# Kernel tuning notes

Measured on AMD Instinct MI355X. Metric: run time of the kernel, lower is better.

## Reference

```python
import jax, jax.numpy as jnp
import numpy as np

N = 100000
E = 1600000
IN_C = 128
HID_C = 128
OUT_C = 128


def sage_conv(x, edge_index, W_l, b_l, W_r):
    # PyG SAGEConv (mean aggr): out = mean_{j in N(i)} x_j @ W_l^T + b_l + x_i @ W_r^T
    src, dst = edge_index[0], edge_index[1]
    n = x.shape[0]
    msgs = x[src]                                            # [E, d] gather
    summed = jax.ops.segment_sum(msgs, dst, num_segments=n)  # [N, d]
    deg = jax.ops.segment_sum(jnp.ones((src.shape[0],), x.dtype), dst, num_segments=n)
    mean = summed / jnp.maximum(deg, 1.0)[:, None]
    return mean @ W_l.T + b_l + x @ W_r.T


def setup_inputs() -> dict:
    key = jax.random.key(0)
    ks = jax.random.split(key, 8)
    x = jax.random.normal(ks[0], (N, IN_C), dtype=jnp.float32)
    edge_index = jax.random.randint(ks[1], (2, E), 0, N, dtype=jnp.int64)
    s1 = 1.0 / np.sqrt(IN_C)
    s2 = 1.0 / np.sqrt(HID_C)
    W1_l = jax.random.uniform(ks[2], (HID_C, IN_C), jnp.float32, -s1, s1)
    b1 = jax.random.uniform(ks[3], (HID_C,), jnp.float32, -s1, s1)
    W1_r = jax.random.uniform(ks[4], (HID_C, IN_C), jnp.float32, -s1, s1)
    W2_l = jax.random.uniform(ks[5], (OUT_C, HID_C), jnp.float32, -s2, s2)
    b2 = jax.random.uniform(ks[6], (OUT_C,), jnp.float32, -s2, s2)
    W2_r = jax.random.uniform(ks[7], (OUT_C, HID_C), jnp.float32, -s2, s2)
    return {"x": x, "edge_index": edge_index, "W1_l": W1_l, "b1": b1, "W1_r": W1_r,
            "W2_l": W2_l, "b2": b2, "W2_r": W2_r}


def reference(x, edge_index, W1_l, b1, W1_r, W2_l, b2, W2_r):
    h = sage_conv(x, edge_index, W1_l, b1, W1_r)
    h = jax.nn.relu(h)
    # F.dropout(p=0.4, training=self.training): identity in eval mode
    out = sage_conv(h, edge_index, W2_l, b2, W2_r)
    return out
```

## Files before the change

kernel.cpp:

```cpp
#include <hip/hip_runtime.h>

#define N_NODES 100000
#define N_EDGES 1600000
#define C 128
#define SCAN_B 1024
#define LDW 264

#define BSH 7
#define NBUCK 782
#define BCAP 2560
#define TILE1 8192
#define NBLK1 196

typedef __attribute__((ext_vector_type(8))) short bfrag;
typedef __attribute__((ext_vector_type(4))) float f32x4;

__device__ __forceinline__ ushort f2b(float x) {
    uint u = __builtin_bit_cast(uint, x);
    u += 0x7fffu + ((u >> 16) & 1u);
    return (ushort)(u >> 16);
}
__device__ __forceinline__ float b2f(ushort b) {
    uint u = ((uint)b) << 16;
    return __builtin_bit_cast(float, u);
}


__global__ __launch_bounds__(256) void bucket_scatter2_k(
        const int* __restrict__ ei, uint* __restrict__ buck, int* __restrict__ bcur) {
    __shared__ int hist[NBUCK];
    __shared__ int base_l[NBUCK];
    int t = threadIdx.x;
    int tile0 = blockIdx.x * TILE1;

    for (int i = t; i < NBUCK; i += 256) hist[i] = 0;
    __syncthreads();
    #pragma unroll 4
    for (int j = 0; j < TILE1 / 256; ++j) {
        int e = tile0 + j * 256 + t;
        if (e < N_EDGES) atomicAdd(&hist[ei[N_EDGES + e] >> BSH], 1);
    }
    __syncthreads();
    for (int i = t; i < NBUCK; i += 256) {
        int h = hist[i];
        base_l[i] = h ? atomicAdd(&bcur[i], h) : 0;
    }
    __syncthreads();
    for (int i = t; i < NBUCK; i += 256) hist[i] = 0;
    __syncthreads();
    #pragma unroll 4
    for (int j = 0; j < TILE1 / 256; ++j) {
        int e = tile0 + j * 256 + t;
        if (e < N_EDGES) {
            int src = ei[e];
            int dst = ei[N_EDGES + e];
            int b = dst >> BSH;
            int r = base_l[b] + atomicAdd(&hist[b], 1);
            if (r < BCAP) buck[(uint)b * BCAP + r] = (uint)src | ((uint)(dst & 127) << 17);
        }
    }
}

__global__ __launch_bounds__(256) void bucket_hist2_k(
        const uint* __restrict__ buck, const int* __restrict__ bcur, int* __restrict__ deg) {
    __shared__ int cnt_l[128];
    int b = blockIdx.x, t = threadIdx.x;
    if (t < 128) cnt_l[t] = 0;
    __syncthreads();
    int cnt = min(bcur[b], BCAP);
    const uint* bp = buck + (uint)b * BCAP;
    for (int i = t; i < cnt; i += 256) atomicAdd(&cnt_l[bp[i] >> 17], 1);
    __syncthreads();
    int node = (b << BSH) + t;
    if (t < 128 && node < N_NODES) deg[node] = cnt_l[t];
}

__global__ void scan1_k(const int* __restrict__ deg, int* __restrict__ rowptr,
                        int* __restrict__ bsums) {
    __shared__ int s[256];
    int b = blockIdx.x, t = threadIdx.x;
    int base = b * SCAN_B + t * 4;
    int v[4];
    int sum = 0;
    #pragma unroll
    for (int j = 0; j < 4; ++j) {
        int idx = base + j;
        v[j] = (idx < N_NODES) ? deg[idx] : 0;
        sum += v[j];
    }
    s[t] = sum;
    __syncthreads();
    for (int off = 1; off < 256; off <<= 1) {
        int x = (t >= off) ? s[t - off] : 0;
        __syncthreads();
        s[t] += x;
        __syncthreads();
    }
    int run = (t > 0) ? s[t - 1] : 0;
    #pragma unroll
    for (int j = 0; j < 4; ++j) {
        run += v[j];
        int idx = base + j;
        if (idx < N_NODES) rowptr[idx + 1] = run;
    }
    if (t == 255) bsums[b] = s[255];
}

__global__ void scan2_k(int* __restrict__ bsums, int nb) {
    __shared__ int s[128];
    int t = threadIdx.x;
    s[t] = (t < nb) ? bsums[t] : 0;
    __syncthreads();
    for (int off = 1; off < 128; off <<= 1) {
        int x = (t >= off) ? s[t - off] : 0;
        __syncthreads();
        s[t] += x;
        __syncthreads();
    }
    if (t < nb) bsums[t] = (t > 0) ? s[t - 1] : 0;
}

__global__ void scan3_k(int* __restrict__ rowptr, const int* __restrict__ bsums) {
    int i = blockIdx.x * blockDim.x + threadIdx.x;
    if (i < N_NODES) rowptr[i + 1] += bsums[i / SCAN_B];
    if (i == 0) rowptr[0] = 0;
}

__global__ __launch_bounds__(256) void bucket_place2_k(
        const uint* __restrict__ buck, const int* __restrict__ bcur,
        const int* __restrict__ rowptr, int* __restrict__ col) {
    __shared__ int base_n[129];
    __shared__ int fill_l[128];
    __shared__ int col_l[BCAP];
    int b = blockIdx.x, t = threadIdx.x;
    int node0 = b << BSH;
    if (t <= 128) base_n[t] = rowptr[min(node0 + t, N_NODES)];
    if (t < 128) fill_l[t] = 0;
    __syncthreads();
    int pbase = base_n[0];
    int cnt = min(bcur[b], BCAP);
    const uint* bp = buck + (uint)b * BCAP;
    for (int i = t; i < cnt; i += 256) {
        uint p = bp[i];
        int rel = p >> 17;
        int pos = base_n[rel] + atomicAdd(&fill_l[rel], 1) - pbase;
        if (pos < BCAP) col_l[pos] = (int)(p & 0x1FFFFu);
    }
    __syncthreads();
    int total = min(base_n[128] - pbase, BCAP);
    for (int i = t; i < total; i += 256) col[pbase + i] = col_l[i];
}


__global__ void cast_x_k(const float4* __restrict__ in, ushort4* __restrict__ out) {
    int i = blockIdx.x * blockDim.x + threadIdx.x;
    if (i < N_NODES * C / 4) {
        float4 v = in[i];
        ushort4 o = { f2b(v.x), f2b(v.y), f2b(v.z), f2b(v.w) };
        out[i] = o;
    }
}

__global__ void wprep_k(const float* __restrict__ Wl, const float* __restrict__ Wr,
                        ushort* __restrict__ wcat) {
    int i = blockIdx.x * blockDim.x + threadIdx.x;
    int o = i >> 8, k = i & 255;
    float v = (k < 128) ? Wl[o * 128 + k] : Wr[o * 128 + (k - 128)];
    wcat[i] = f2b(v);
}

__global__ __launch_bounds__(256) void agg_bf16_k(
        const uint* __restrict__ feat,
        uint* __restrict__ outb,
        const int* __restrict__ rowptr, const int* __restrict__ col) {
    int wave = threadIdx.x >> 6, lane = threadIdx.x & 63;
    int node = blockIdx.x * 4 + wave;
    int beg = rowptr[node], end = rowptr[node + 1];
    float a0 = 0.f, a1 = 0.f;
    for (int e0 = beg; e0 < end; e0 += 64) {
        int cnt = min(64, end - e0);
        int cv = col[min(e0 + lane, end - 1)];
        int j = 0;
        for (; j + 8 <= cnt; j += 8) {
            uint v0 = feat[((uint)__shfl(cv, j + 0) << 6) + lane];
            uint v1 = feat[((uint)__shfl(cv, j + 1) << 6) + lane];
            uint v2 = feat[((uint)__shfl(cv, j + 2) << 6) + lane];
            uint v3 = feat[((uint)__shfl(cv, j + 3) << 6) + lane];
            uint v4 = feat[((uint)__shfl(cv, j + 4) << 6) + lane];
            uint v5 = feat[((uint)__shfl(cv, j + 5) << 6) + lane];
            uint v6 = feat[((uint)__shfl(cv, j + 6) << 6) + lane];
            uint v7 = feat[((uint)__shfl(cv, j + 7) << 6) + lane];
            a0 += b2f((ushort)v0) + b2f((ushort)v1) + b2f((ushort)v2) + b2f((ushort)v3)
                + b2f((ushort)v4) + b2f((ushort)v5) + b2f((ushort)v6) + b2f((ushort)v7);
            a1 += b2f((ushort)(v0 >> 16)) + b2f((ushort)(v1 >> 16))
                + b2f((ushort)(v2 >> 16)) + b2f((ushort)(v3 >> 16))
                + b2f((ushort)(v4 >> 16)) + b2f((ushort)(v5 >> 16))
                + b2f((ushort)(v6 >> 16)) + b2f((ushort)(v7 >> 16));
        }
        for (; j < cnt; ++j) {
            uint v = feat[((uint)__shfl(cv, j) << 6) + lane];
            a0 += b2f((ushort)v);
            a1 += b2f((ushort)(v >> 16));
        }
    }
    float inv = 1.f / (float)max(end - beg, 1);
    uint o = (uint)f2b(a0 * inv) | ((uint)f2b(a1 * inv) << 16);
    outb[((uint)node << 6) + lane] = o;
}

template <bool RELU, bool OUT_BF16>
__global__ __launch_bounds__(256) void mfma_lin_k(
        const ushort* __restrict__ A0,
        const ushort* __restrict__ A1,
        const ushort* __restrict__ W,
        const float* __restrict__ bias,
        void* __restrict__ outp) {
    __shared__ ushort wl[128 * LDW];
    int t = threadIdx.x;

    const bfrag* wg = (const bfrag*)W;
    #pragma unroll
    for (int j = 0; j < 16; ++j) {
        int p = t + j * 256;
        int o = p >> 5, kb = p & 31;
        *(bfrag*)&wl[o * LDW + kb * 8] = wg[p];
    }
    __syncthreads();

    int wave = t >> 6, lane = t & 63;
    int g = lane >> 4, r16 = lane & 15;
    long base = (long)blockIdx.x * 128 + wave * 32;

    const ushort* a0p[2];
    const ushort* a1p[2];
    #pragma unroll
    for (int mt = 0; mt < 2; ++mt) {
        long mrow = base + mt * 16 + r16;
        if (mrow >= N_NODES) mrow = N_NODES - 1;
        a0p[mt] = A0 + mrow * C + g * 8;
        a1p[mt] = A1 + mrow * C + g * 8;
    }

    f32x4 acc[2][8];
    #pragma unroll
    for (int mt = 0; mt < 2; ++mt)
        #pragma unroll
        for (int nt = 0; nt < 8; ++nt) acc[mt][nt] = (f32x4){0.f, 0.f, 0.f, 0.f};

    #pragma unroll
    for (int c = 0; c < 8; ++c) {
        bfrag a[2];
        #pragma unroll
        for (int mt = 0; mt < 2; ++mt)
            a[mt] = (c < 4) ? *(const bfrag*)(a0p[mt] + c * 32)
                            : *(const bfrag*)(a1p[mt] + (c - 4) * 32);
        #pragma unroll
        for (int nt = 0; nt < 8; ++nt) {
            bfrag b = *(const bfrag*)&wl[(nt * 16 + r16) * LDW + g * 8 + c * 32];
            acc[0][nt] = __builtin_amdgcn_mfma_f32_16x16x32_bf16(a[0], b, acc[0][nt], 0, 0, 0);
            acc[1][nt] = __builtin_amdgcn_mfma_f32_16x16x32_bf16(a[1], b, acc[1][nt], 0, 0, 0);
        }
    }

    #pragma unroll
    for (int nt = 0; nt < 8; ++nt) {
        int o = nt * 16 + r16;
        float bv = bias[o];
        #pragma unroll
        for (int mt = 0; mt < 2; ++mt) {
            #pragma unroll
            for (int i = 0; i < 4; ++i) {
                long orow = base + mt * 16 + g * 4 + i;
                if (orow < N_NODES) {
                    float v = acc[mt][nt][i] + bv;
                    if (RELU) v = fmaxf(v, 0.f);
                    if (OUT_BF16)
                        ((ushort*)outp)[orow * C + o] = f2b(v);
                    else
                        ((float*)outp)[orow * C + o] = v;
                }
            }
        }
    }
}

extern "C" void kernel_launch(void* const* d_in, const int* in_sizes, int n_in,
                              void* d_out, int out_size, void* d_ws, size_t ws_size,
                              hipStream_t stream) {
    const float* x   = (const float*)d_in[0];
    const int* ei    = (const int*)d_in[1];
    const float* W1l = (const float*)d_in[2];
    const float* b1  = (const float*)d_in[3];
    const float* W1r = (const float*)d_in[4];
    const float* W2l = (const float*)d_in[5];
    const float* b2  = (const float*)d_in[6];
    const float* W2r = (const float*)d_in[7];
    float* out       = (float*)d_out;

    char* ws = (char*)d_ws;
    size_t off = 0;
    ushort* xb    = (ushort*)(ws + off); off += (size_t)N_NODES * C * 2;
    ushort* aggb  = (ushort*)(ws + off); off += (size_t)N_NODES * C * 2;
    ushort* hb    = (ushort*)(ws + off); off += (size_t)N_NODES * C * 2;
    uint* buck    = (uint*)hb;
    ushort* wcat1 = (ushort*)(ws + off); off += (size_t)C * 256 * 2;
    ushort* wcat2 = (ushort*)(ws + off); off += (size_t)C * 256 * 2;
    int* col      = (int*)(ws + off);    off += (size_t)N_EDGES * 4;
    int* rowptr   = (int*)(ws + off);    off += (size_t)(N_NODES + 1) * 4;
    int* deg      = (int*)(ws + off);    off += (size_t)NBUCK * 128 * 4;
    int* bcur     = (int*)(ws + off);    off += 1024 * 4;
    int* bsums    = (int*)(ws + off);    off += 1024 * 4;

    int nb = (N_NODES + SCAN_B - 1) / SCAN_B;

    hipMemsetAsync(bcur, 0, 1024 * 4, stream);
    bucket_scatter2_k<<<NBLK1, 256, 0, stream>>>(ei, buck, bcur);
    bucket_hist2_k<<<NBUCK, 256, 0, stream>>>(buck, bcur, deg);
    scan1_k<<<nb, 256, 0, stream>>>(deg, rowptr, bsums);
    scan2_k<<<1, 128, 0, stream>>>(bsums, nb);
    scan3_k<<<(N_NODES + 255) / 256, 256, 0, stream>>>(rowptr, bsums);
    bucket_place2_k<<<NBUCK, 256, 0, stream>>>(buck, bcur, rowptr, col);

    cast_x_k<<<(N_NODES * C / 4 + 255) / 256, 256, 0, stream>>>((const float4*)x, (ushort4*)xb);
    wprep_k<<<128, 256, 0, stream>>>(W1l, W1r, wcat1);
    wprep_k<<<128, 256, 0, stream>>>(W2l, W2r, wcat2);

    int lin_blocks = (N_NODES + 127) / 128;

    agg_bf16_k<<<N_NODES / 4, 256, 0, stream>>>((const uint*)xb, (uint*)aggb, rowptr, col);
    mfma_lin_k<true, true><<<lin_blocks, 256, 0, stream>>>(aggb, xb, wcat1, b1, hb);

    agg_bf16_k<<<N_NODES / 4, 256, 0, stream>>>((const uint*)hb, (uint*)aggb, rowptr, col);
    mfma_lin_k<false, false><<<lin_blocks, 256, 0, stream>>>(aggb, hb, wcat2, b2, out);
}
```

Before: 260.3 us.

## Split bf16 features into 8 column slabs so gathers stay cache-resident

Stores node features in a slab-major layout of eight 16-column slices, each 32 bytes per node, and runs aggregation once per slab. Each wave now gathers 8 neighbors at a time with 8 lanes per row, then reduces with cross-lane shuffles. The intent is for each slab's working set (about 3.2 MB) to fit in L2, so random neighbor gathers hit cache instead of HBM. In exchange there are 8x more blocks, col and rowptr are re-read once per slab, each gather is a short 32-byte segment, and the MFMA linear kernel has to read and write the new layout.

```diff
diff --git a/kernel.cpp b/kernel.cpp
--- a/kernel.cpp
+++ b/kernel.cpp
@@ -24,6 +24,7 @@
     uint u = ((uint)b) << 16;
     return __builtin_bit_cast(float, u);
 }
+
 
 
 __global__ __launch_bounds__(256) void bucket_scatter2_k(
@@ -152,12 +153,14 @@
 }
 
 
-__global__ void cast_x_k(const float4* __restrict__ in, ushort4* __restrict__ out) {
+__global__ void cast_x_sm_k(const float* __restrict__ in, uint* __restrict__ out) {
     int i = blockIdx.x * blockDim.x + threadIdx.x;
-    if (i < N_NODES * C / 4) {
-        float4 v = in[i];
-        ushort4 o = { f2b(v.x), f2b(v.y), f2b(v.z), f2b(v.w) };
-        out[i] = o;
+    if (i < N_NODES * 64) {
+        int s = i / (N_NODES * 8);
+        int rem = i - s * (N_NODES * 8);
+        int n = rem >> 3, u = rem & 7;
+        const float* p = in + n * C + s * 16 + u * 2;
+        out[i] = (uint)f2b(p[0]) | ((uint)f2b(p[1]) << 16);
     }
 }
 
@@ -169,49 +172,44 @@
     wcat[i] = f2b(v);
 }
 
-__global__ __launch_bounds__(256) void agg_bf16_k(
+__global__ __launch_bounds__(256) void agg_sm_k(
         const uint* __restrict__ feat,
         uint* __restrict__ outb,
         const int* __restrict__ rowptr, const int* __restrict__ col) {
     int wave = threadIdx.x >> 6, lane = threadIdx.x & 63;
-    int node = blockIdx.x * 4 + wave;
+    int s = blockIdx.x & 7;
+    int node = (blockIdx.x >> 3) * 4 + wave;
+    const uint* fs = feat + ((uint)s * N_NODES << 3);
     int beg = rowptr[node], end = rowptr[node + 1];
+    int grp = lane >> 3, u = lane & 7;
     float a0 = 0.f, a1 = 0.f;
     for (int e0 = beg; e0 < end; e0 += 64) {
-        int cnt = min(64, end - e0);
-        int cv = col[min(e0 + lane, end - 1)];
-        int j = 0;
-        for (; j + 8 <= cnt; j += 8) {
-            uint v0 = feat[((uint)__shfl(cv, j + 0) << 6) + lane];
-            uint v1 = feat[((uint)__shfl(cv, j + 1) << 6) + lane];
-            uint v2 = feat[((uint)__shfl(cv, j + 2) << 6) + lane];
-            uint v3 = feat[((uint)__shfl(cv, j + 3) << 6) + lane];
-            uint v4 = feat[((uint)__shfl(cv, j + 4) << 6) + lane];
-            uint v5 = feat[((uint)__shfl(cv, j + 5) << 6) + lane];
-            uint v6 = feat[((uint)__shfl(cv, j + 6) << 6) + lane];
-            uint v7 = feat[((uint)__shfl(cv, j + 7) << 6) + lane];
-            a0 += b2f((ushort)v0) + b2f((ushort)v1) + b2f((ushort)v2) + b2f((ushort)v3)
-                + b2f((ushort)v4) + b2f((ushort)v5) + b2f((ushort)v6) + b2f((ushort)v7);
-            a1 += b2f((ushort)(v0 >> 16)) + b2f((ushort)(v1 >> 16))
-                + b2f((ushort)(v2 >> 16)) + b2f((ushort)(v3 >> 16))
-                + b2f((ushort)(v4 >> 16)) + b2f((ushort)(v5 >> 16))
-                + b2f((ushort)(v6 >> 16)) + b2f((ushort)(v7 >> 16));
+        int cv = __builtin_nontemporal_load(&col[min(e0 + lane, end - 1)]);
+        int nit = min(64, end - e0);
+        for (int it = 0; it < nit; it += 16) {
+            int i0 = it + grp, i1 = it + 8 + grp;
+            int s0 = __shfl(cv, i0);
+            int s1 = __shfl(cv, i1);
+            uint f0 = fs[((uint)s0 << 3) + u];
+            uint f1 = fs[((uint)s1 << 3) + u];
+            if (i0 < nit) { a0 += b2f((ushort)f0); a1 += b2f((ushort)(f0 >> 16)); }
+            if (i1 < nit) { a0 += b2f((ushort)f1); a1 += b2f((ushort)(f1 >> 16)); }
         }
-        for (; j < cnt; ++j) {
-            uint v = feat[((uint)__shfl(cv, j) << 6) + lane];
-            a0 += b2f((ushort)v);
-            a1 += b2f((ushort)(v >> 16));
-        }
-    }
-    float inv = 1.f / (float)max(end - beg, 1);
-    uint o = (uint)f2b(a0 * inv) | ((uint)f2b(a1 * inv) << 16);
-    outb[((uint)node << 6) + lane] = o;
+    }
+    a0 += __shfl_xor(a0, 8);  a1 += __shfl_xor(a1, 8);
+    a0 += __shfl_xor(a0, 16); a1 += __shfl_xor(a1, 16);
+    a0 += __shfl_xor(a0, 32); a1 += __shfl_xor(a1, 32);
+    if (lane < 8) {
+        float inv = 1.f / (float)max(end - beg, 1);
+        uint o = (uint)f2b(a0 * inv) | ((uint)f2b(a1 * inv) << 16);
+        __builtin_nontemporal_store(o, &outb[(((uint)s * N_NODES + (uint)node) << 3) + u]);
+    }
 }
 
 template <bool RELU, bool OUT_BF16>
 __global__ __launch_bounds__(256) void mfma_lin_k(
-        const ushort* __restrict__ A0,
-        const ushort* __restrict__ A1,
+        const uint* __restrict__ A0,
+        const uint* __restrict__ A1,
         const ushort* __restrict__ W,
         const float* __restrict__ bias,
         void* __restrict__ outp) {
@@ -231,15 +229,15 @@
     int g = lane >> 4, r16 = lane & 15;
     long base = (long)blockIdx.x * 128 + wave * 32;
 
-    const ushort* a0p[2];
-    const ushort* a1p[2];
+    uint mr[2];
     #pragma unroll
     for (int mt = 0; mt < 2; ++mt) {
         long mrow = base + mt * 16 + r16;
         if (mrow >= N_NODES) mrow = N_NODES - 1;
-        a0p[mt] = A0 + mrow * C + g * 8;
-        a1p[mt] = A1 + mrow * C + g * 8;
-    }
+        mr[mt] = (uint)mrow;
+    }
+    uint su = (uint)(g >> 1);
+    uint u0 = (uint)(g & 1) * 4;
 
     f32x4 acc[2][8];
     #pragma unroll
@@ -249,11 +247,12 @@
 
     #pragma unroll
     for (int c = 0; c < 8; ++c) {
+        const uint* bp = (c < 4) ? A0 : A1;
+        uint sidx = (uint)(c < 4 ? 2 * c : 2 * (c - 4)) + su;
         bfrag a[2];
         #pragma unroll
         for (int mt = 0; mt < 2; ++mt)
-            a[mt] = (c < 4) ? *(const bfrag*)(a0p[mt] + c * 32)
-                            : *(const bfrag*)(a1p[mt] + (c - 4) * 32);
+            a[mt] = *(const bfrag*)(bp + (((sidx * N_NODES + mr[mt]) << 3) + u0));
         #pragma unroll
         for (int nt = 0; nt < 8; ++nt) {
             bfrag b = *(const bfrag*)&wl[(nt * 16 + r16) * LDW + g * 8 + c * 32];
@@ -275,7 +274,7 @@
                     float v = acc[mt][nt][i] + bv;
                     if (RELU) v = fmaxf(v, 0.f);
                     if (OUT_BF16)
-                        ((ushort*)outp)[orow * C + o] = f2b(v);
+                        ((ushort*)outp)[(((uint)nt * N_NODES + (uint)orow) << 4) + r16] = f2b(v);
                     else
                         ((float*)outp)[orow * C + o] = v;
                 }
@@ -299,10 +298,10 @@
 
     char* ws = (char*)d_ws;
     size_t off = 0;
-    ushort* xb    = (ushort*)(ws + off); off += (size_t)N_NODES * C * 2;
-    ushort* aggb  = (ushort*)(ws + off); off += (size_t)N_NODES * C * 2;
-    ushort* hb    = (ushort*)(ws + off); off += (size_t)N_NODES * C * 2;
-    uint* buck    = (uint*)hb;
+    uint* xb      = (uint*)(ws + off);   off += (size_t)N_NODES * C * 2;
+    uint* aggb    = (uint*)(ws + off);   off += (size_t)N_NODES * C * 2;
+    uint* hb      = (uint*)(ws + off);   off += (size_t)N_NODES * C * 2;
+    uint* buck    = hb;
     ushort* wcat1 = (ushort*)(ws + off); off += (size_t)C * 256 * 2;
     ushort* wcat2 = (ushort*)(ws + off); off += (size_t)C * 256 * 2;
     int* col      = (int*)(ws + off);    off += (size_t)N_EDGES * 4;
@@ -321,15 +320,16 @@
     scan3_k<<<(N_NODES + 255) / 256, 256, 0, stream>>>(rowptr, bsums);
     bucket_place2_k<<<NBUCK, 256, 0, stream>>>(buck, bcur, rowptr, col);
 
-    cast_x_k<<<(N_NODES * C / 4 + 255) / 256, 256, 0, stream>>>((const float4*)x, (ushort4*)xb);
+    cast_x_sm_k<<<(N_NODES * 64 + 255) / 256, 256, 0, stream>>>(x, xb);
     wprep_k<<<128, 256, 0, stream>>>(W1l, W1r, wcat1);
     wprep_k<<<128, 256, 0, stream>>>(W2l, W2r, wcat2);
 
     int lin_blocks = (N_NODES + 127) / 128;
-
-    agg_bf16_k<<<N_NODES / 4, 256, 0, stream>>>((const uint*)xb, (uint*)aggb, rowptr, col);
+    int agg_blocks = (N_NODES / 4) * 8;
+
+    agg_sm_k<<<agg_blocks, 256, 0, stream>>>(xb, aggb, rowptr, col);
     mfma_lin_k<true, true><<<lin_blocks, 256, 0, stream>>>(aggb, xb, wcat1, b1, hb);
 
-    agg_bf16_k<<<N_NODES / 4, 256, 0, stream>>>((const uint*)hb, (uint*)aggb, rowptr, col);
+    agg_sm_k<<<agg_blocks, 256, 0, stream>>>(hb, aggb, rowptr, col);
     mfma_lin_k<false, false><<<lin_blocks, 256, 0, stream>>>(aggb, hb, wcat2, b2, out);
 }
```

Result: slower. 587.0 us (+125.5%).

## Aggregate neighbor features via MFMA with one-hot selection matrices over 16-node groups

Applied to the files above, without the earlier changes.

Each wave now handles 16 consecutive destination nodes. It gathers their combined edge list in chunks of 32, stages the neighbor rows transposed in LDS, and sums them with bf16 MFMA against a one-hot matrix that marks each edge's destination row. The local destination index is packed into the upper bits of col during CSR placement so the wave can build that matrix. The aim is to replace per-lane scalar bf16 unpack-and-add work with matrix instructions and to use wider gathers. The cost is more LDS traffic and transposes, and wasted MFMA work on the zero entries of the one-hot matrix.

```diff
diff --git a/kernel.cpp b/kernel.cpp
--- a/kernel.cpp
+++ b/kernel.cpp
@@ -19,10 +19,6 @@
     uint u = __builtin_bit_cast(uint, x);
     u += 0x7fffu + ((u >> 16) & 1u);
     return (ushort)(u >> 16);
-}
-__device__ __forceinline__ float b2f(ushort b) {
-    uint u = ((uint)b) << 16;
-    return __builtin_bit_cast(float, u);
 }
 
 
@@ -144,7 +140,7 @@
         uint p = bp[i];
         int rel = p >> 17;
         int pos = base_n[rel] + atomicAdd(&fill_l[rel], 1) - pbase;
-        if (pos < BCAP) col_l[pos] = (int)(p & 0x1FFFFu);
+        if (pos < BCAP) col_l[pos] = (int)((p & 0x1FFFFu) | (((uint)rel & 15u) << 17));
     }
     __syncthreads();
     int total = min(base_n[128] - pbase, BCAP);
@@ -169,43 +165,80 @@
     wcat[i] = f2b(v);
 }
 
-__global__ __launch_bounds__(256) void agg_bf16_k(
+__global__ __launch_bounds__(256) void agg_mfma_k(
         const uint* __restrict__ feat,
-        uint* __restrict__ outb,
+        ushort* __restrict__ outb,
         const int* __restrict__ rowptr, const int* __restrict__ col) {
+    __shared__ uint et[4][64 * 33];
+    __shared__ ushort pb[4][64 * 8];
     int wave = threadIdx.x >> 6, lane = threadIdx.x & 63;
-    int node = blockIdx.x * 4 + wave;
-    int beg = rowptr[node], end = rowptr[node + 1];
-    float a0 = 0.f, a1 = 0.f;
-    for (int e0 = beg; e0 < end; e0 += 64) {
-        int cnt = min(64, end - e0);
-        int cv = col[min(e0 + lane, end - 1)];
-        int j = 0;
-        for (; j + 8 <= cnt; j += 8) {
-            uint v0 = feat[((uint)__shfl(cv, j + 0) << 6) + lane];
-            uint v1 = feat[((uint)__shfl(cv, j + 1) << 6) + lane];
-            uint v2 = feat[((uint)__shfl(cv, j + 2) << 6) + lane];
-            uint v3 = feat[((uint)__shfl(cv, j + 3) << 6) + lane];
-            uint v4 = feat[((uint)__shfl(cv, j + 4) << 6) + lane];
-            uint v5 = feat[((uint)__shfl(cv, j + 5) << 6) + lane];
-            uint v6 = feat[((uint)__shfl(cv, j + 6) << 6) + lane];
-            uint v7 = feat[((uint)__shfl(cv, j + 7) << 6) + lane];
-            a0 += b2f((ushort)v0) + b2f((ushort)v1) + b2f((ushort)v2) + b2f((ushort)v3)
-                + b2f((ushort)v4) + b2f((ushort)v5) + b2f((ushort)v6) + b2f((ushort)v7);
-            a1 += b2f((ushort)(v0 >> 16)) + b2f((ushort)(v1 >> 16))
-                + b2f((ushort)(v2 >> 16)) + b2f((ushort)(v3 >> 16))
-                + b2f((ushort)(v4 >> 16)) + b2f((ushort)(v5 >> 16))
-                + b2f((ushort)(v6 >> 16)) + b2f((ushort)(v7 >> 16));
-        }
-        for (; j < cnt; ++j) {
-            uint v = feat[((uint)__shfl(cv, j) << 6) + lane];
-            a0 += b2f((ushort)v);
-            a1 += b2f((ushort)(v >> 16));
-        }
-    }
-    float inv = 1.f / (float)max(end - beg, 1);
-    uint o = (uint)f2b(a0 * inv) | ((uint)f2b(a1 * inv) << 16);
-    outb[((uint)node << 6) + lane] = o;
+    int n0 = (blockIdx.x * 4 + wave) * 16;
+    int m = lane & 15, g = lane >> 4;
+
+    int rp = rowptr[min(n0 + min(lane, 16), N_NODES)];
+    int beg = __shfl(rp, 0), end = __shfl(rp, 16);
+    int degm = __shfl(rp, m + 1) - __shfl(rp, m);
+    float invdeg = 1.0f / (float)max(degm, 1);
+
+    uint* etw = et[wave];
+    ushort* pbw = pb[wave];
+    uint sel = (m & 1) ? 0x07060302u : 0x05040100u;
+
+    f32x4 acc[8];
+    #pragma unroll
+    for (int t = 0; t < 8; ++t) acc[t] = (f32x4){0.f, 0.f, 0.f, 0.f};
+
+    for (int e0 = beg; e0 < end; e0 += 32) {
+        int cnt = min(32, end - e0);
+        int cv = col[e0 + min(lane & 31, cnt - 1)];
+
+        *(bfrag*)&pbw[lane * 8] = (bfrag){0, 0, 0, 0, 0, 0, 0, 0};
+        if (lane < cnt) {
+            int dr = (cv >> 17) & 15;
+            pbw[((lane >> 3) * 16 + dr) * 8 + (lane & 7)] = 0x3F80;
+        }
+
+        #pragma unroll
+        for (int q = 0; q < 16; ++q) {
+            int r = 2 * q + (lane >> 5);
+            uint src = (uint)__shfl(cv, r) & 0x1FFFFu;
+            uint2 v = *(const uint2*)(feat + ((size_t)src << 6) + 2 * (lane & 31));
+            int uch = 2 * (lane & 31);
+            etw[uch * 33 + r] = v.x;
+            etw[(uch + 1) * 33 + r] = v.y;
+        }
+        asm volatile("s_waitcnt lgkmcnt(0)" ::: "memory");
+
+        bfrag bf = *(const bfrag*)&pbw[lane * 8];
+        #pragma unroll
+        for (int t = 0; t < 8; ++t) {
+            const uint* ap = etw + (8 * t + (m >> 1)) * 33 + 8 * g;
+            uint u0 = ap[0], u1 = ap[1], u2 = ap[2], u3 = ap[3];
+            uint u4 = ap[4], u5 = ap[5], u6 = ap[6], u7 = ap[7];
+            uint4 av = { __builtin_amdgcn_perm(u1, u0, sel),
+                         __builtin_amdgcn_perm(u3, u2, sel),
+                         __builtin_amdgcn_perm(u5, u4, sel),
+                         __builtin_amdgcn_perm(u7, u6, sel) };
+            bfrag af = __builtin_bit_cast(bfrag, av);
+            acc[t] = __builtin_amdgcn_mfma_f32_16x16x32_bf16(af, bf, acc[t], 0, 0, 0);
+        }
+    }
+
+    ushort* ol = (ushort*)etw;
+    #pragma unroll
+    for (int t = 0; t < 8; ++t)
+        #pragma unroll
+        for (int i = 0; i < 4; ++i)
+            ol[m * 136 + t * 16 + g * 4 + i] = f2b(acc[t][i] * invdeg);
+    asm volatile("s_waitcnt lgkmcnt(0)" ::: "memory");
+    #pragma unroll
+    for (int q = 0; q < 4; ++q) {
+        int row = (q * 64 + lane) >> 4;
+        int node = n0 + row;
+        uint4 vv = *(const uint4*)&ol[row * 136 + (lane & 15) * 8];
+        if (node < N_NODES)
+            *(uint4*)&outb[(size_t)node * 128 + (lane & 15) * 8] = vv;
+    }
 }
 
 template <bool RELU, bool OUT_BF16>
@@ -326,10 +359,11 @@
     wprep_k<<<128, 256, 0, stream>>>(W2l, W2r, wcat2);
 
     int lin_blocks = (N_NODES + 127) / 128;
-
-    agg_bf16_k<<<N_NODES / 4, 256, 0, stream>>>((const uint*)xb, (uint*)aggb, rowptr, col);
+    int agg_blocks = (N_NODES + 63) / 64;
+
+    agg_mfma_k<<<agg_blocks, 256, 0, stream>>>((const uint*)xb, aggb, rowptr, col);
     mfma_lin_k<true, true><<<lin_blocks, 256, 0, stream>>>(aggb, xb, wcat1, b1, hb);
 
-    agg_bf16_k<<<N_NODES / 4, 256, 0, stream>>>((const uint*)hb, (uint*)aggb, rowptr, col);
+    agg_mfma_k<<<agg_blocks, 256, 0, stream>>>((const uint*)hb, aggb, rowptr, col);
     mfma_lin_k<false, false><<<lin_blocks, 256, 0, stream>>>(aggb, hb, wcat2, b2, out);
 }
```

Result: slower. 300.8 us (+15.6%).
